# Kernel tuning notes

Hardware: AMD Instinct MI355X
Metric: run time of the kernel (lower is better)

## Reference

```python
import jax, jax.numpy as jnp
import numpy as np

B, C, H, W = 64, 64, 32, 32
K = 1024  # codebook_num
EPS = 1e-10


def setup_inputs() -> dict:
    key = jax.random.key(0)
    kz, kc = jax.random.split(key)
    z = jax.random.normal(kz, (B, C, H, W), dtype=jnp.float32)
    # nn.init.uniform_(codebook.weight, -1/K, 1/K)
    codebook = jax.random.uniform(kc, (K, C), dtype=jnp.float32, minval=-1.0 / K, maxval=1.0 / K)
    return {"z": z, "codebook": codebook}


def reference(z, codebook):
    Bz, Cz, Hz, Wz = z.shape
    flat_z = jnp.transpose(z, (0, 2, 3, 1)).reshape(-1, Cz)  # [N, C]
    dists = (jnp.sum(flat_z ** 2, axis=1, keepdims=True)
             + jnp.sum(codebook ** 2, axis=1)
             - 2.0 * flat_z @ codebook.T)
    indices = jnp.argmin(dists, axis=1)  # [N] int
    quantized_z = codebook[indices].reshape(Bz, Hz, Wz, Cz).transpose(0, 3, 1, 2)
    quantized_z_st = z + jax.lax.stop_gradient(quantized_z - z)
    # perplexity: probs = mean one-hot = histogram / N
    n = indices.shape[0]
    counts = jax.ops.segment_sum(jnp.ones((n,), dtype=jnp.float32), indices, num_segments=K)
    probs = counts / n
    perplexity = jnp.exp(-jnp.sum(probs * jnp.log(jnp.clip(probs, EPS))))
    return quantized_z, quantized_z_st, indices, perplexity
```

## Files before the change

### kernel.cpp

```cpp
#include <hip/hip_runtime.h>
#include <math.h>

#define NVEC   65536
#define CDIM   64
#define KBOOK  1024
#define NTOT   4194304


typedef __bf16 bf16x8 __attribute__((ext_vector_type(8)));
typedef float  f32x4  __attribute__((ext_vector_type(4)));

__global__ void prep_kernel(const float* __restrict__ cb, float* __restrict__ se,
                            int* __restrict__ hist, __bf16* __restrict__ cbT) {
    const int t = blockIdx.x * 256 + threadIdx.x;
    hist[t] = 0;
    const float* row = cb + t * CDIM;
    float r[8];
#pragma unroll
    for (int j = 0; j < 8; ++j) r[j] = __fmul_rn(row[j], row[j]);
#pragma unroll
    for (int i = 8; i < 64; i += 8)
#pragma unroll
        for (int j = 0; j < 8; ++j) r[j] = __fadd_rn(r[j], __fmul_rn(row[i + j], row[i + j]));
    se[t] = __fadd_rn(__fadd_rn(__fadd_rn(r[0], r[1]), __fadd_rn(r[2], r[3])),
                      __fadd_rn(__fadd_rn(r[4], r[5]), __fadd_rn(r[6], r[7])));
    const int tt = t >> 4, la = t & 15;
    __bf16* tb = cbT + (size_t)tt * 2048;
#pragma unroll
    for (int g = 0; g < 4; ++g)
#pragma unroll
        for (int j = 0; j < 8; ++j) {
            const float e0 = row[8 * g + j];
            const float e1 = row[32 + 8 * g + j];
            const __bf16 h0 = (__bf16)e0, h1 = (__bf16)e1;
            const int lo8 = (g * 16 + la) * 8 + j;
            tb[lo8]              = h0;
            tb[512 + lo8]        = h1;
            tb[1024 + lo8]       = (__bf16)(e0 - (float)h0);
            tb[1536 + lo8]       = (__bf16)(e1 - (float)h1);
        }
}

__launch_bounds__(256)
__attribute__((amdgpu_waves_per_eu(4, 4)))
__global__ void approx_kernel(const float* __restrict__ z, const __bf16* __restrict__ cbT,
                              const float* __restrict__ se,
                              unsigned int* __restrict__ cand) {
    const int tid = threadIdx.x;
    const int w = tid >> 6;
    const int l = tid & 63;
    const int la = l & 15;
    const int g  = l >> 4;
    const int n = blockIdx.x * 64 + w * 16 + la;
    const int b = n >> 10, hw = n & 1023;
    const float* zb = z + (size_t)b * (CDIM * 1024) + hw;

    bf16x8 mh0, ml0, mh1, ml1;
#pragma unroll
    for (int j = 0; j < 8; ++j) {
        {
            float zc = zb[(g * 8 + j) * 1024];
            float m  = -2.0f * zc;
            __bf16 h = (__bf16)m;
            mh0[j] = h; ml0[j] = (__bf16)(m - (float)h);
        }
        {
            float zc = zb[(32 + g * 8 + j) * 1024];
            float m  = -2.0f * zc;
            __bf16 h = (__bf16)m;
            mh1[j] = h; ml1[j] = (__bf16)(m - (float)h);
        }
    }

    float b1 = 3.4e38f, b2 = 3.4e38f;
    int   k1 = 0,       k2 = 0;
    const int kv = g * 4;
    const __bf16* tbase = cbT + (size_t)l * 8;

#define DECL_SLOT(s) bf16x8 ah0_##s, ah1_##s, al0_##s, al1_##s; f32x4 se_##s;
    DECL_SLOT(a) DECL_SLOT(b)
#undef DECL_SLOT

#define LOADT(s, ttv) { const int t_ = (ttv) & 63;                       \
        const __bf16* p_ = tbase + (size_t)t_ * 2048;                    \
        ah0_##s = *(const bf16x8*)(p_);                                  \
        ah1_##s = *(const bf16x8*)(p_ + 512);                            \
        al0_##s = *(const bf16x8*)(p_ + 1024);                           \
        al1_##s = *(const bf16x8*)(p_ + 1536);                           \
        se_##s  = *(const f32x4*)(se + t_ * 16 + kv); }

#define INS1(d_, kt_) { const bool c1 = (d_) < b1, c2 = (d_) < b2;       \
        b2 = c1 ? b1 : (c2 ? (d_) : b2);  k2 = c1 ? k1 : (c2 ? (kt_) : k2); \
        b1 = c1 ? (d_) : b1;              k1 = c1 ? (kt_) : k1; }

#define COMPT(s, ttv) { const int k0_ = (ttv) * 16;                      \
        f32x4 aA = se_##s; f32x4 aB = {0.f, 0.f, 0.f, 0.f};              \
        aA = __builtin_amdgcn_mfma_f32_16x16x32_bf16(ah0_##s, mh0, aA, 0, 0, 0); \
        aB = __builtin_amdgcn_mfma_f32_16x16x32_bf16(ah1_##s, mh1, aB, 0, 0, 0); \
        aA = __builtin_amdgcn_mfma_f32_16x16x32_bf16(al0_##s, mh0, aA, 0, 0, 0); \
        aB = __builtin_amdgcn_mfma_f32_16x16x32_bf16(al1_##s, mh1, aB, 0, 0, 0); \
        aA = __builtin_amdgcn_mfma_f32_16x16x32_bf16(ah0_##s, ml0, aA, 0, 0, 0); \
        aB = __builtin_amdgcn_mfma_f32_16x16x32_bf16(ah1_##s, ml1, aB, 0, 0, 0); \
        { const float d0_ = aA[0] + aB[0]; INS1(d0_, k0_ + kv)     }     \
        { const float d1_ = aA[1] + aB[1]; INS1(d1_, k0_ + kv + 1) }     \
        { const float d2_ = aA[2] + aB[2]; INS1(d2_, k0_ + kv + 2) }     \
        { const float d3_ = aA[3] + aB[3]; INS1(d3_, k0_ + kv + 3) } }

    LOADT(a, 0)
    for (int tt = 0; tt < 64; tt += 2) {
        LOADT(b, tt + 1)
        COMPT(a, tt)
        LOADT(a, tt + 2)
        COMPT(b, tt + 1)
    }
#undef LOADT
#undef INS1
#undef COMPT

    cand[n * 4 + g] = (unsigned int)k1 | ((unsigned int)k2 << 16);
}

__global__ void rescore_kernel(const float* __restrict__ z, const float* __restrict__ cb,
                               const float* __restrict__ se,
                               const unsigned int* __restrict__ cand,
                               unsigned long long* __restrict__ keys) {
    const int n = blockIdx.x * 256 + threadIdx.x;
    int ks[8];
#pragma unroll
    for (int g = 0; g < 4; ++g) {
        const unsigned int p = cand[n * 4 + g];
        ks[2 * g]     = (int)(p & 0xFFFFu);
        ks[2 * g + 1] = (int)(p >> 16);
    }
    const int b = n >> 10, hw = n & 1023;
    const float* zb = z + (size_t)b * (CDIM * 1024) + hw;

    float zx[64], r[8];
#pragma unroll
    for (int j = 0; j < 8; ++j) {
        const float zc = zb[j * 1024];
        zx[j] = zc + zc;
        r[j] = __fmul_rn(zc, zc);
    }
#pragma unroll
    for (int c = 8; c < 64; ++c) {
        const float zc = zb[c * 1024];
        zx[c] = zc + zc;
        r[c & 7] = __fadd_rn(r[c & 7], __fmul_rn(zc, zc));
    }
    const float sx = __fadd_rn(__fadd_rn(__fadd_rn(r[0], r[1]), __fadd_rn(r[2], r[3])),
                               __fadd_rn(__fadd_rn(r[4], r[5]), __fadd_rn(r[6], r[7])));

    float a[8];
#pragma unroll
    for (int i = 0; i < 8; ++i) a[i] = 0.0f;
    const float4* cb4 = (const float4*)cb;
#pragma unroll
    for (int q = 0; q < 16; ++q) {
#pragma unroll
        for (int i = 0; i < 8; ++i) {
            const float4 ev = cb4[ks[i] * 16 + q];
            a[i] = fmaf(zx[4 * q],     ev.x, a[i]);
            a[i] = fmaf(zx[4 * q + 1], ev.y, a[i]);
            a[i] = fmaf(zx[4 * q + 2], ev.z, a[i]);
            a[i] = fmaf(zx[4 * q + 3], ev.w, a[i]);
        }
    }
    unsigned long long best = ~0ull;
#pragma unroll
    for (int i = 0; i < 8; ++i) {
        const float d = __fsub_rn(__fadd_rn(sx, se[ks[i]]), a[i]);
        unsigned int ob = __float_as_uint(d);
        ob = (ob & 0x80000000u) ? ~ob : (ob | 0x80000000u);
        const unsigned long long key = ((unsigned long long)ob << 32) | (unsigned int)ks[i];
        if (key < best) best = key;
    }
    keys[n] = best;
}

__global__ void scatter_kernel(const float* __restrict__ z, const float* __restrict__ cb,
                               const unsigned long long* __restrict__ keys,
                               float* __restrict__ out) {
    const int o = (blockIdx.x * 256 + threadIdx.x) * 4;
    const int b = o >> 16, c = (o >> 10) & 63, hw = o & 1023;
    const int n = (b << 10) | hw;
    float q[4];
#pragma unroll
    for (int j = 0; j < 4; ++j) {
        const int k = (int)(keys[n + j] & 0xFFFFFFFFu);
        q[j] = cb[k * CDIM + c];
    }
    const float4 zv = *(const float4*)(z + o);
    *(float4*)(out + o) = make_float4(q[0], q[1], q[2], q[3]);
    float4 st;
    st.x = __fadd_rn(zv.x, __fsub_rn(q[0], zv.x));
    st.y = __fadd_rn(zv.y, __fsub_rn(q[1], zv.y));
    st.z = __fadd_rn(zv.z, __fsub_rn(q[2], zv.z));
    st.w = __fadd_rn(zv.w, __fsub_rn(q[3], zv.w));
    *(float4*)(out + NTOT + o) = st;
}

__global__ void hist_kernel(const unsigned long long* __restrict__ keys, int* __restrict__ hist,
                            float* __restrict__ outIdxF) {
    __shared__ int lh[KBOOK];
    for (int i = threadIdx.x; i < KBOOK; i += 256) lh[i] = 0;
    __syncthreads();
    const int n = blockIdx.x * 256 + threadIdx.x;
    const int k = (int)(keys[n] & 0xFFFFFFFFu);
    outIdxF[n] = (float)k;
    atomicAdd(&lh[k], 1);
    __syncthreads();
    for (int i = threadIdx.x; i < KBOOK; i += 256)
        if (lh[i]) atomicAdd(&hist[i], lh[i]);
}

__global__ void perp_kernel(const int* __restrict__ hist, float* __restrict__ out) {
    __shared__ double partial[16];
    const int t = threadIdx.x;
    const int c = hist[t];
    double term = 0.0;
    if (c > 0) { double p = (double)c / (double)NVEC; term = p * log(p); }
    for (int off = 32; off > 0; off >>= 1) term += __shfl_down(term, off);
    if ((t & 63) == 0) partial[t >> 6] = term;
    __syncthreads();
    if (t == 0) {
        double s = 0.0;
        for (int i = 0; i < 16; ++i) s += partial[i];
        out[2 * NTOT + NVEC] = (float)exp(-s);
    }
}

extern "C" void kernel_launch(void* const* d_in, const int* in_sizes, int n_in,
                              void* d_out, int out_size, void* d_ws, size_t ws_size,
                              hipStream_t stream) {
    const float* z  = (const float*)d_in[0];
    const float* cb = (const float*)d_in[1];
    float* out = (float*)d_out;

    char* ws = (char*)d_ws;
    unsigned long long* keys = (unsigned long long*)(ws + 0);
    float* se   = (float*)(ws + 524288);
    int*   hist = (int*)(ws + 528384);

    char* outB = (char*)d_out;
    unsigned int* cand = (unsigned int*)(outB);
    __bf16* cbT = (__bf16*)(outB + (1 << 20));

    prep_kernel<<<4, 256, 0, stream>>>(cb, se, hist, cbT);
    approx_kernel<<<NVEC / 64, 256, 0, stream>>>(z, cbT, se, cand);
    rescore_kernel<<<NVEC / 256, 256, 0, stream>>>(z, cb, se, cand, keys);
    scatter_kernel<<<NTOT / 1024, 256, 0, stream>>>(z, cb, keys, out);
    hist_kernel<<<NVEC / 256, 256, 0, stream>>>(keys, hist, out + 2 * NTOT);
    perp_kernel<<<1, 1024, 0, stream>>>(hist, out);
}
```

Measured before the change: 182.1 us.

## Fuse histogram into rescore, perplexity into scatter, deepen approx prefetch

Moves the histogram and index-float output into the rescore kernel and folds the perplexity reduction into block 0 of the scatter kernel, removing two kernel launches and a reread of the keys. The approx kernel's software pipeline goes from two to four register slots, so more codebook tiles are in flight per iteration. The deeper prefetch raises register pressure and could reduce occupancy. The perplexity work now sits on one scatter block, which adds a serial tail to that block.

```diff
diff --git a/kernel.cpp b/kernel.cpp
--- a/kernel.cpp
+++ b/kernel.cpp
@@ -78,7 +78,7 @@
     const __bf16* tbase = cbT + (size_t)l * 8;
 
 #define DECL_SLOT(s) bf16x8 ah0_##s, ah1_##s, al0_##s, al1_##s; f32x4 se_##s;
-    DECL_SLOT(a) DECL_SLOT(b)
+    DECL_SLOT(a) DECL_SLOT(b) DECL_SLOT(c) DECL_SLOT(d)
 #undef DECL_SLOT
 
 #define LOADT(s, ttv) { const int t_ = (ttv) & 63;                       \
@@ -106,12 +106,12 @@
         { const float d2_ = aA[2] + aB[2]; INS1(d2_, k0_ + kv + 2) }     \
         { const float d3_ = aA[3] + aB[3]; INS1(d3_, k0_ + kv + 3) } }
 
-    LOADT(a, 0)
-    for (int tt = 0; tt < 64; tt += 2) {
-        LOADT(b, tt + 1)
-        COMPT(a, tt)
-        LOADT(a, tt + 2)
-        COMPT(b, tt + 1)
+    LOADT(a, 0) LOADT(b, 1)
+    for (int tt = 0; tt < 64; tt += 4) {
+        LOADT(c, tt + 2) LOADT(d, tt + 3)
+        COMPT(a, tt)     COMPT(b, tt + 1)
+        LOADT(a, tt + 4) LOADT(b, tt + 5)
+        COMPT(c, tt + 2) COMPT(d, tt + 3)
     }
 #undef LOADT
 #undef INS1
@@ -123,7 +123,12 @@
 __global__ void rescore_kernel(const float* __restrict__ z, const float* __restrict__ cb,
                                const float* __restrict__ se,
                                const unsigned int* __restrict__ cand,
-                               unsigned long long* __restrict__ keys) {
+                               unsigned long long* __restrict__ keys,
+                               int* __restrict__ hist, float* __restrict__ outIdxF) {
+    __shared__ int lh[KBOOK];
+    for (int i = threadIdx.x; i < KBOOK; i += 256) lh[i] = 0;
+    __syncthreads();
+
     const int n = blockIdx.x * 256 + threadIdx.x;
     int ks[8];
 #pragma unroll
@@ -176,10 +181,17 @@
         if (key < best) best = key;
     }
     keys[n] = best;
+    const int kbest = (int)(best & 0xFFFFFFFFu);
+    outIdxF[n] = (float)kbest;
+    atomicAdd(&lh[kbest], 1);
+    __syncthreads();
+    for (int i = threadIdx.x; i < KBOOK; i += 256)
+        if (lh[i]) atomicAdd(&hist[i], lh[i]);
 }
 
 __global__ void scatter_kernel(const float* __restrict__ z, const float* __restrict__ cb,
                                const unsigned long long* __restrict__ keys,
+                               const int* __restrict__ hist,
                                float* __restrict__ out) {
     const int o = (blockIdx.x * 256 + threadIdx.x) * 4;
     const int b = o >> 16, c = (o >> 10) & 63, hw = o & 1023;
@@ -198,35 +210,23 @@
     st.z = __fadd_rn(zv.z, __fsub_rn(q[2], zv.z));
     st.w = __fadd_rn(zv.w, __fsub_rn(q[3], zv.w));
     *(float4*)(out + NTOT + o) = st;
-}
-
-__global__ void hist_kernel(const unsigned long long* __restrict__ keys, int* __restrict__ hist,
-                            float* __restrict__ outIdxF) {
-    __shared__ int lh[KBOOK];
-    for (int i = threadIdx.x; i < KBOOK; i += 256) lh[i] = 0;
-    __syncthreads();
-    const int n = blockIdx.x * 256 + threadIdx.x;
-    const int k = (int)(keys[n] & 0xFFFFFFFFu);
-    outIdxF[n] = (float)k;
-    atomicAdd(&lh[k], 1);
-    __syncthreads();
-    for (int i = threadIdx.x; i < KBOOK; i += 256)
-        if (lh[i]) atomicAdd(&hist[i], lh[i]);
-}
-
-__global__ void perp_kernel(const int* __restrict__ hist, float* __restrict__ out) {
-    __shared__ double partial[16];
-    const int t = threadIdx.x;
-    const int c = hist[t];
-    double term = 0.0;
-    if (c > 0) { double p = (double)c / (double)NVEC; term = p * log(p); }
-    for (int off = 32; off > 0; off >>= 1) term += __shfl_down(term, off);
-    if ((t & 63) == 0) partial[t >> 6] = term;
-    __syncthreads();
-    if (t == 0) {
-        double s = 0.0;
-        for (int i = 0; i < 16; ++i) s += partial[i];
-        out[2 * NTOT + NVEC] = (float)exp(-s);
+
+    if (blockIdx.x == 0) {
+        __shared__ double partial[4];
+        const int t = threadIdx.x;
+        double term = 0.0;
+#pragma unroll
+        for (int j = 0; j < 4; ++j) {
+            const int cnt = hist[t + 256 * j];
+            if (cnt > 0) { const double p = (double)cnt / (double)NVEC; term += p * log(p); }
+        }
+        for (int off = 32; off > 0; off >>= 1) term += __shfl_down(term, off);
+        if ((t & 63) == 0) partial[t >> 6] = term;
+        __syncthreads();
+        if (t == 0) {
+            const double s = partial[0] + partial[1] + partial[2] + partial[3];
+            out[2 * NTOT + NVEC] = (float)exp(-s);
+        }
     }
 }
 
@@ -248,8 +248,6 @@
 
     prep_kernel<<<4, 256, 0, stream>>>(cb, se, hist, cbT);
     approx_kernel<<<NVEC / 64, 256, 0, stream>>>(z, cbT, se, cand);
-    rescore_kernel<<<NVEC / 256, 256, 0, stream>>>(z, cb, se, cand, keys);
-    scatter_kernel<<<NTOT / 1024, 256, 0, stream>>>(z, cb, keys, out);
-    hist_kernel<<<NVEC / 256, 256, 0, stream>>>(keys, hist, out + 2 * NTOT);
-    perp_kernel<<<1, 1024, 0, stream>>>(hist, out);
-}
+    rescore_kernel<<<NVEC / 256, 256, 0, stream>>>(z, cb, se, cand, keys, hist, out + 2 * NTOT);
+    scatter_kernel<<<NTOT / 1024, 256, 0, stream>>>(z, cb, keys, hist, out);
+}
```

Result: faster. 173.6 us (-4.7%).
